# Kernel tuning notes

Measured on AMD Instinct MI355X. Metric: run time of the kernel, lower is better.

Reference implementation:

```python
import jax, jax.numpy as jnp
import numpy as np

B, D_IN, D_OUT = 131072, 256, 256

def setup_inputs() -> dict:
    key = jax.random.key(0)
    k1, k2, k3 = jax.random.split(key, 3)
    x = jax.random.normal(k1, (B, D_IN), dtype=jnp.float32)
    # One weight row / bias scalar per SingleNeuron, concatenated: [D_OUT, D_IN], [D_OUT]
    bound = 1.0 / np.sqrt(D_IN)  # nn.Linear default init scale
    W = jax.random.uniform(k2, (D_OUT, D_IN), dtype=jnp.float32, minval=-bound, maxval=bound)
    b = jax.random.uniform(k3, (D_OUT,), dtype=jnp.float32, minval=-bound, maxval=bound)
    return {"x": x, "W": W, "b": b}

def reference(x, W, b):
    # Fused equivalent of looping per-neuron Linear(in,1), stack(dim=1), squeeze, relu
    return jax.nn.relu(jnp.einsum('bi,oi->bo', x, W) + b)
```

## Files before the change

### kernel.cpp

```cpp
#include <hip/hip_runtime.h>


#define BM 128
#define BN 128

typedef __attribute__((ext_vector_type(16))) float f32x16;
typedef __attribute__((ext_vector_type(8))) __bf16 bf16x8;

__device__ __forceinline__ void cvt8(const float4& A, const float4& B,
                                     bf16x8& hi, bf16x8& lo) {
    const float f[8] = {A.x, A.y, A.z, A.w, B.x, B.y, B.z, B.w};
#pragma unroll
    for (int j = 0; j < 8; ++j) {
        const unsigned int u = __builtin_bit_cast(unsigned int, f[j]);
        hi[j] = __builtin_bit_cast(__bf16, (unsigned short)(u >> 16));
        const float hf = __builtin_bit_cast(float, u & 0xffff0000u);
        const float lf = f[j] - hf;
        lo[j] = __builtin_bit_cast(__bf16,
                    (unsigned short)(__builtin_bit_cast(unsigned int, lf) >> 16));
    }
}

#define MFMA(a, b, c) \
    (c) = __builtin_amdgcn_mfma_f32_32x32x16_bf16((a), (b), (c), 0, 0, 0)

__global__ __launch_bounds__(256)
void gemm_mfma_kernel(const float* __restrict__ x,
                      const float* __restrict__ W,
                      const float* __restrict__ bias,
                      float* __restrict__ out) {
    const int tid  = threadIdx.x;
    const int lane = tid & 63;
    const int wid  = tid >> 6;
    const int wm   = wid >> 1;
    const int wn   = wid & 1;
    const int rt   = (int)(blockIdx.x >> 1);
    const int ct   = (int)(blockIdx.x & 1);

    const int r31 = lane & 31;
    const int g   = lane >> 5;

    const long arow = (long)rt * BM + wm * 64 + r31;
    const int  bcol = ct * BN + wn * 64 + r31;
    const float* ap0 = x + arow * 256 + g * 8;
    const float* ap1 = ap0 + 32 * 256;
    const float* bp0 = W + (long)bcol * 256 + g * 8;
    const float* bp1 = bp0 + 32 * 256;

    f32x16 acc[2][2];
#pragma unroll
    for (int i = 0; i < 2; ++i)
#pragma unroll
        for (int j = 0; j < 2; ++j)
#pragma unroll
            for (int r = 0; r < 16; ++r) acc[i][j][r] = 0.f;

    float4 a0A = *(const float4*)(ap0);
    float4 a0B = *(const float4*)(ap0 + 4);
    float4 a1A = *(const float4*)(ap1);
    float4 a1B = *(const float4*)(ap1 + 4);
    float4 b0A = *(const float4*)(bp0);
    float4 b0B = *(const float4*)(bp0 + 4);
    float4 b1A = *(const float4*)(bp1);
    float4 b1B = *(const float4*)(bp1 + 4);

#pragma unroll
    for (int t = 0; t < 16; ++t) {
        bf16x8 ah0, al0, ah1, al1, bh0, bl0, bh1, bl1;
        cvt8(a0A, a0B, ah0, al0);
        cvt8(a1A, a1B, ah1, al1);
        cvt8(b0A, b0B, bh0, bl0);
        cvt8(b1A, b1B, bh1, bl1);

        if (t < 15) {
            const int o = (t + 1) * 16;
            a0A = *(const float4*)(ap0 + o);
            a0B = *(const float4*)(ap0 + o + 4);
            a1A = *(const float4*)(ap1 + o);
            a1B = *(const float4*)(ap1 + o + 4);
            b0A = *(const float4*)(bp0 + o);
            b0B = *(const float4*)(bp0 + o + 4);
            b1A = *(const float4*)(bp1 + o);
            b1B = *(const float4*)(bp1 + o + 4);
        }

        MFMA(ah0, bh0, acc[0][0]); MFMA(ah0, bh1, acc[0][1]);
        MFMA(ah1, bh0, acc[1][0]); MFMA(ah1, bh1, acc[1][1]);
        MFMA(ah0, bl0, acc[0][0]); MFMA(ah0, bl1, acc[0][1]);
        MFMA(ah1, bl0, acc[1][0]); MFMA(ah1, bl1, acc[1][1]);
        MFMA(al0, bh0, acc[0][0]); MFMA(al0, bh1, acc[0][1]);
        MFMA(al1, bh0, acc[1][0]); MFMA(al1, bh1, acc[1][1]);
    }

    const int  ocol0 = ct * BN + wn * 64;
    const long orow0 = (long)rt * BM + wm * 64;
    const float bj0 = bias[ocol0 + r31];
    const float bj1 = bias[ocol0 + 32 + r31];

#pragma unroll
    for (int i = 0; i < 2; ++i) {
#pragma unroll
        for (int r = 0; r < 16; ++r) {
            const int rowf = (r & 3) + 8 * (r >> 2) + 4 * g;
            const long row = orow0 + i * 32 + rowf;
            float v0 = acc[i][0][r] + bj0;
            float v1 = acc[i][1][r] + bj1;
            v0 = v0 > 0.f ? v0 : 0.f;
            v1 = v1 > 0.f ? v1 : 0.f;
            out[row * 256 + ocol0 + r31]      = v0;
            out[row * 256 + ocol0 + 32 + r31] = v1;
        }
    }
}

extern "C" void kernel_launch(void* const* d_in, const int* in_sizes, int n_in,
                              void* d_out, int out_size, void* d_ws, size_t ws_size,
                              hipStream_t stream) {
    (void)n_in; (void)d_ws; (void)ws_size; (void)out_size;
    const float* x = (const float*)d_in[0];
    const float* W = (const float*)d_in[1];
    const float* b = (const float*)d_in[2];
    float* out = (float*)d_out;

    const int M = in_sizes[0] / 256;
    const int grid = (M / BM) * 2;

    gemm_mfma_kernel<<<grid, 256, 0, stream>>>(x, W, b, out);
}
```

Measured before the change: 314.6 us.

## Stage x tiles via LDS double buffering and pre-split W to bf16

Adds a small pre-kernel that splits W once into hi/lo bf16 fragments laid out in MFMA order, so the main kernel loads them directly instead of converting per block. x tiles are staged into XOR-swizzled shared memory with global_load_lds and double buffered across 8 K-chunks, and block indices are swizzled for cache locality. This aims to cut redundant W conversion and improve x load coalescing, at the cost of barriers, LDS use, an extra launch, and a swizzle that hardcodes the grid size.

```diff
diff --git a/kernel.cpp b/kernel.cpp
--- a/kernel.cpp
+++ b/kernel.cpp
@@ -1,11 +1,11 @@
 #include <hip/hip_runtime.h>
 
 
-#define BM 128
-#define BN 128
-
 typedef __attribute__((ext_vector_type(16))) float f32x16;
 typedef __attribute__((ext_vector_type(8))) __bf16 bf16x8;
+
+#define MFMA(a, b, c) \
+    (c) = __builtin_amdgcn_mfma_f32_32x32x16_bf16((a), (b), (c), 0, 0, 0)
 
 __device__ __forceinline__ void cvt8(const float4& A, const float4& B,
                                      bf16x8& hi, bf16x8& lo) {
@@ -21,31 +21,58 @@
     }
 }
 
-#define MFMA(a, b, c) \
-    (c) = __builtin_amdgcn_mfma_f32_32x32x16_bf16((a), (b), (c), 0, 0, 0)
+__device__ __forceinline__ void gload16(const float* g, float* l) {
+    __builtin_amdgcn_global_load_lds(
+        (const __attribute__((address_space(1))) void*)g,
+        (__attribute__((address_space(3))) void*)l, 16, 0, 0);
+}
+
+__global__ __launch_bounds__(256)
+void wprep_kernel(const float* __restrict__ W,
+                  __bf16* __restrict__ whi, __bf16* __restrict__ wlo) {
+    const int wv = (int)blockIdx.x * 4 + (threadIdx.x >> 6);
+    const int l  = threadIdx.x & 63;
+    const int t  = wv & 15;
+    const int j  = (wv >> 4) & 1;
+    const int wn = (wv >> 5) & 1;
+    const int ct = wv >> 6;
+    const int n  = ct * 128 + wn * 64 + j * 32 + (l & 31);
+    const int k  = t * 16 + (l >> 5) * 8;
+    const float4 A = *(const float4*)(W + n * 256 + k);
+    const float4 B = *(const float4*)(W + n * 256 + k + 4);
+    bf16x8 hi, lo;
+    cvt8(A, B, hi, lo);
+    *(bf16x8*)(whi + wv * 512 + l * 8) = hi;
+    *(bf16x8*)(wlo + wv * 512 + l * 8) = lo;
+}
 
 __global__ __launch_bounds__(256)
 void gemm_mfma_kernel(const float* __restrict__ x,
-                      const float* __restrict__ W,
+                      const __bf16* __restrict__ whi,
+                      const __bf16* __restrict__ wlo,
                       const float* __restrict__ bias,
                       float* __restrict__ out) {
+    __shared__ float xs[2][4096];
+
     const int tid  = threadIdx.x;
     const int lane = tid & 63;
     const int wid  = tid >> 6;
     const int wm   = wid >> 1;
     const int wn   = wid & 1;
-    const int rt   = (int)(blockIdx.x >> 1);
-    const int ct   = (int)(blockIdx.x & 1);
+
+    const int bid = (int)blockIdx.x;
+    const int swz = (bid & 7) * 256 + (bid >> 3);
+    const int rt  = swz >> 1;
+    const int ct  = swz & 1;
 
     const int r31 = lane & 31;
     const int g   = lane >> 5;
+    const long row0 = (long)rt * 128;
 
-    const long arow = (long)rt * BM + wm * 64 + r31;
-    const int  bcol = ct * BN + wn * 64 + r31;
-    const float* ap0 = x + arow * 256 + g * 8;
-    const float* ap1 = ap0 + 32 * 256;
-    const float* bp0 = W + (long)bcol * 256 + g * 8;
-    const float* bp1 = bp0 + 32 * 256;
+    const int Gbase = wid * 64 + lane;
+    const int m0 = wm * 64 + r31;
+    const int m1 = m0 + 32;
+    const int sw = r31 & 7;
 
     f32x16 acc[2][2];
 #pragma unroll
@@ -55,45 +82,65 @@
 #pragma unroll
             for (int r = 0; r < 16; ++r) acc[i][j][r] = 0.f;
 
-    float4 a0A = *(const float4*)(ap0);
-    float4 a0B = *(const float4*)(ap0 + 4);
-    float4 a1A = *(const float4*)(ap1);
-    float4 a1B = *(const float4*)(ap1 + 4);
-    float4 b0A = *(const float4*)(bp0);
-    float4 b0B = *(const float4*)(bp0 + 4);
-    float4 b1A = *(const float4*)(bp1);
-    float4 b1B = *(const float4*)(bp1 + 4);
+    const int fbase0 = (ct * 4 + wn * 2) * 16;
+    const __bf16* whip = whi + (long)lane * 8;
+    const __bf16* wlop = wlo + (long)lane * 8;
 
+    auto STAGE = [&](int b, int chunk) {
 #pragma unroll
-    for (int t = 0; t < 16; ++t) {
-        bf16x8 ah0, al0, ah1, al1, bh0, bl0, bh1, bl1;
-        cvt8(a0A, a0B, ah0, al0);
-        cvt8(a1A, a1B, ah1, al1);
-        cvt8(b0A, b0B, bh0, bl0);
-        cvt8(b1A, b1B, bh1, bl1);
+        for (int j = 0; j < 4; ++j) {
+            const int G = j * 256 + Gbase;
+            const int m = G >> 3;
+            const int cs = (G & 7) ^ (m & 7);
+            const float* gp = x + (row0 + m) * 256 + chunk * 32 + cs * 4;
+            float* lp = &xs[b][(j * 256 + wid * 64) * 4];
+            gload16(gp, lp);
+        }
+    };
 
-        if (t < 15) {
-            const int o = (t + 1) * 16;
-            a0A = *(const float4*)(ap0 + o);
-            a0B = *(const float4*)(ap0 + o + 4);
-            a1A = *(const float4*)(ap1 + o);
-            a1B = *(const float4*)(ap1 + o + 4);
-            b0A = *(const float4*)(bp0 + o);
-            b0B = *(const float4*)(bp0 + o + 4);
-            b1A = *(const float4*)(bp1 + o);
-            b1B = *(const float4*)(bp1 + o + 4);
+    auto COMPUTE = [&](int b, int chunk) {
+#pragma unroll
+        for (int t = 0; t < 2; ++t) {
+            const int ks = chunk * 2 + t;
+            const int c0 = t * 4 + g * 2;
+            const float* xb = &xs[b][0];
+            const float4 A0a = *(const float4*)(xb + m0 * 32 + ((c0 ^ sw) * 4));
+            const float4 A0b = *(const float4*)(xb + m0 * 32 + (((c0 + 1) ^ sw) * 4));
+            const float4 A1a = *(const float4*)(xb + m1 * 32 + ((c0 ^ sw) * 4));
+            const float4 A1b = *(const float4*)(xb + m1 * 32 + (((c0 + 1) ^ sw) * 4));
+            bf16x8 ah0, al0, ah1, al1;
+            cvt8(A0a, A0b, ah0, al0);
+            cvt8(A1a, A1b, ah1, al1);
+
+            const long f0 = (long)(fbase0 + ks) * 512;
+            const long f1 = f0 + 16 * 512;
+            const bf16x8 bh0 = *(const bf16x8*)(whip + f0);
+            const bf16x8 bl0 = *(const bf16x8*)(wlop + f0);
+            const bf16x8 bh1 = *(const bf16x8*)(whip + f1);
+            const bf16x8 bl1 = *(const bf16x8*)(wlop + f1);
+
+            MFMA(ah0, bh0, acc[0][0]); MFMA(ah0, bh1, acc[0][1]);
+            MFMA(ah1, bh0, acc[1][0]); MFMA(ah1, bh1, acc[1][1]);
+            MFMA(ah0, bl0, acc[0][0]); MFMA(ah0, bl1, acc[0][1]);
+            MFMA(ah1, bl0, acc[1][0]); MFMA(ah1, bl1, acc[1][1]);
+            MFMA(al0, bh0, acc[0][0]); MFMA(al0, bh1, acc[0][1]);
+            MFMA(al1, bh0, acc[1][0]); MFMA(al1, bh1, acc[1][1]);
         }
+    };
 
-        MFMA(ah0, bh0, acc[0][0]); MFMA(ah0, bh1, acc[0][1]);
-        MFMA(ah1, bh0, acc[1][0]); MFMA(ah1, bh1, acc[1][1]);
-        MFMA(ah0, bl0, acc[0][0]); MFMA(ah0, bl1, acc[0][1]);
-        MFMA(ah1, bl0, acc[1][0]); MFMA(ah1, bl1, acc[1][1]);
-        MFMA(al0, bh0, acc[0][0]); MFMA(al0, bh1, acc[0][1]);
-        MFMA(al1, bh0, acc[1][0]); MFMA(al1, bh1, acc[1][1]);
+    STAGE(0, 0);
+    asm volatile("s_waitcnt vmcnt(0)" ::: "memory");
+    __syncthreads();
+    for (int c = 0; c < 7; ++c) {
+        STAGE((c + 1) & 1, c + 1);
+        COMPUTE(c & 1, c);
+        asm volatile("s_waitcnt vmcnt(0)" ::: "memory");
+        __syncthreads();
     }
+    COMPUTE(1, 7);
 
-    const int  ocol0 = ct * BN + wn * 64;
-    const long orow0 = (long)rt * BM + wm * 64;
+    const int  ocol0 = ct * 128 + wn * 64;
+    const long orow0 = (long)rt * 128 + wm * 64;
     const float bj0 = bias[ocol0 + r31];
     const float bj1 = bias[ocol0 + 32 + r31];
 
@@ -116,14 +163,18 @@
 extern "C" void kernel_launch(void* const* d_in, const int* in_sizes, int n_in,
                               void* d_out, int out_size, void* d_ws, size_t ws_size,
                               hipStream_t stream) {
-    (void)n_in; (void)d_ws; (void)ws_size; (void)out_size;
+    (void)n_in; (void)ws_size; (void)out_size;
     const float* x = (const float*)d_in[0];
     const float* W = (const float*)d_in[1];
     const float* b = (const float*)d_in[2];
     float* out = (float*)d_out;
 
+    __bf16* whi = (__bf16*)d_ws;
+    __bf16* wlo = whi + 65536;
+
+    wprep_kernel<<<32, 256, 0, stream>>>(W, whi, wlo);
+
     const int M = in_sizes[0] / 256;
-    const int grid = (M / BM) * 2;
-
-    gemm_mfma_kernel<<<grid, 256, 0, stream>>>(x, W, b, out);
+    const int grid = (M / 128) * 2;
+    gemm_mfma_kernel<<<grid, 256, 0, stream>>>(x, whi, wlo, b, out);
 }
```

New measurement: 262.0 us. -16.7%, faster.
